# Performance work log

Measured on AMD Instinct MI355X. Metric: run time of the kernel, lower is better.

Reference implementation:

```python
import jax, jax.numpy as jnp
import numpy as np

KERNEL = 3
PAD = KERNEL // 2  # 1


def cal_wfft_ortho(weight, n, cout, cin):
    # weight: [N, M, k, k] with M < N
    nf = n // 2 + 1
    vfft = jnp.fft.rfft2(weight, s=(n, n), norm='ortho')          # [N, M, n, nf] complex
    vfft = jnp.transpose(vfft, (2, 3, 0, 1))                       # [n, nf, N, M]
    vH = jnp.conj(jnp.swapaxes(vfft, -1, -2))                      # [n, nf, M, N]
    wfft = vH @ vfft                                               # [n, nf, M, M] Gram
    perturb_ratio = 1e-5
    eps = jnp.mean(jnp.diagonal(wfft, axis1=-2, axis2=-1), axis=-1) * perturb_ratio
    m = wfft.shape[-1]
    wfft = wfft + eps[..., None, None] * jnp.eye(m, dtype=wfft.dtype)
    N = vfft.shape[-2]
    I = jnp.eye(N, dtype=wfft.dtype)
    # Cayley-style orthogonal projector: I - 2 V (V^H V)^{-1} V^H
    ortho = I - 2.0 * (vfft @ jnp.linalg.solve(wfft, vH))          # [n, nf, N, N]
    ortho = ortho[:, :, :cout, :cin]
    return ortho.reshape(n * nf, cout, cin)


def setup_inputs() -> dict:
    key = jax.random.key(0)
    k1, k2, k3 = jax.random.split(key, 3)
    B, C, H = 64, 256, 32
    x = jax.random.normal(k1, (B, C, H, H), dtype=jnp.float32)
    # masked low-rank orthogonal weight: [cout, cin-1, 3, 3]
    weight = jax.random.normal(k2, (C, C - 1, KERNEL, KERNEL), dtype=jnp.float32) * 0.05
    bias = jax.random.normal(k3, (C,), dtype=jnp.float32) * 0.01
    return {"x": x, "weight": weight, "bias": bias}


def reference(x, weight, bias):
    B, cin, h, _ = x.shape
    cout = weight.shape[0]
    xp = jnp.pad(x, ((0, 0), (0, 0), (PAD, PAD), (PAD, PAD)))
    n = h + 2 * PAD
    nf = n // 2 + 1
    # x to frequency domain: [n*nf, cin, B]
    xfft = jnp.fft.rfft2(xp, norm='ortho')                         # [B, cin, n, nf]
    xfft = jnp.transpose(xfft, (2, 3, 1, 0)).reshape(n * nf, cin, B)
    W = cal_wfft_ortho(weight, n, cout, cin)                       # [n*nf, cout, cin]
    zfft = W @ xfft                                                # [n*nf, cout, B]
    zfft = jnp.transpose(zfft.reshape(n, nf, cout, B), (3, 2, 0, 1))
    z = jnp.fft.irfft2(zfft, norm='ortho')                         # [B, cout, n, n] real
    z = z[:, :, PAD:-PAD, PAD:-PAD]
    z = z + bias[:, None, None]
    return z
```

## Files before the change

kernel.cpp:

```cpp
#include <hip/hip_runtime.h>
#include <math.h>

#define NN    34
#define NFH   18
#define NFREQ 612
#define CH    256
#define CIN   255
#define NB    64
#define HW    32
#define PI2   6.2831853071795864769f
#define TSTRIDE 36864

__device__ __forceinline__ int tIdx(int I, int J){ return ((I*(I+1))>>1) + J; }

__global__ __launch_bounds__(256) void kF1(const float* __restrict__ x, float2* __restrict__ U){
  __shared__ float tc[NFH][HW], ts[NFH][HW];
  int tid = threadIdx.x;
  for (int i = tid; i < NFH*HW; i += 256){
    int kx = i >> 5, w = i & 31;
    float s, c; sincosf(-PI2*(float)(kx*(w+1))/34.f, &s, &c);
    tc[kx][w] = c; ts[kx][w] = s;
  }
  __syncthreads();
  int c = blockIdx.x;
  int a = (blockIdx.y << 2) + (tid >> 6);
  int b = tid & 63;
  const float4* xr = (const float4*)(x + (((size_t)b*CH + c)*HW + a)*HW);
  float xv[HW];
#pragma unroll
  for (int t = 0; t < 8; t++){
    float4 v = xr[t];
    xv[4*t] = v.x; xv[4*t+1] = v.y; xv[4*t+2] = v.z; xv[4*t+3] = v.w;
  }
#pragma unroll 1
  for (int kx = 0; kx < NFH; kx++){
    float re = 0.f, im = 0.f;
#pragma unroll
    for (int w = 0; w < HW; w++){ re += xv[w]*tc[kx][w]; im += xv[w]*ts[kx][w]; }
    U[(((size_t)a*NFH + kx)*CH + c)*NB + b] = make_float2(re, im);
  }
}

__global__ __launch_bounds__(512) void kF2(const float2* __restrict__ U, float2* __restrict__ X){
  __shared__ float pc[NN][HW], ps[NN][HW];
  int tid = threadIdx.x;
  for (int i = tid; i < NN*HW; i += 512){
    int ky = i >> 5, a = i & 31;
    float s, c; sincosf(-PI2*(float)(ky*(a+1))/34.f, &s, &c);
    pc[ky][a] = c*(1.f/34.f); ps[ky][a] = s*(1.f/34.f);
  }
  __syncthreads();
  int kx = blockIdx.x;
  int c  = (blockIdx.y << 3) + (tid >> 6);
  int b  = tid & 63;
  float2 u[HW];
#pragma unroll
  for (int a = 0; a < HW; a++) u[a] = U[(((size_t)a*NFH + kx)*CH + c)*NB + b];
#pragma unroll 1
  for (int ky = 0; ky < NN; ky++){
    float re = 0.f, im = 0.f;
#pragma unroll
    for (int a = 0; a < HW; a++){
      float cc = pc[ky][a], ss = ps[ky][a];
      re += u[a].x*cc - u[a].y*ss;
      im += u[a].x*ss + u[a].y*cc;
    }
    X[(((size_t)ky*NFH + kx)*CH + c)*NB + b] = make_float2(re, im);
  }
}

__global__ __launch_bounds__(256) void kT0(const float* __restrict__ w, float* __restrict__ wT){
  int idx = blockIdx.x*256 + threadIdx.x;
  if (idx >= 9*CH*CIN) return;
  int k = idx / (CH*CIN);
  int r = idx - k*(CH*CIN);
  wT[idx] = w[(size_t)r*9 + k];
}

__global__ __launch_bounds__(256) void kC(const float* __restrict__ wT, float* __restrict__ C2){
  int kk = blockIdx.x;
  int k1 = kk / 9, k2 = kk - k1*9;
  int to = (blockIdx.y >> 2) << 6, tp = (blockIdx.y & 3) << 6;
  __shared__ float As[64][33], Bs[64][33];
  int tid = threadIdx.x;
  int ty = tid >> 4, tx = tid & 15;
  float acc[4][4] = {};
  const float* Ab = wT + (size_t)k1*CH*CIN;
  const float* Bb = wT + (size_t)k2*CH*CIN;
  for (int i0 = 0; i0 < CIN; i0 += 32){
    for (int idx = tid; idx < 64*32; idx += 256){
      int r = idx >> 5, j = idx & 31;
      int i = i0 + j;
      As[r][j] = (i < CIN) ? Ab[(size_t)(to + r)*CIN + i] : 0.f;
      Bs[r][j] = (i < CIN) ? Bb[(size_t)(tp + r)*CIN + i] : 0.f;
    }
    __syncthreads();
#pragma unroll
    for (int j = 0; j < 32; j++){
      float av[4], bv[4];
#pragma unroll
      for (int d = 0; d < 4; d++){ av[d] = As[ty*4+d][j]; bv[d] = Bs[tx*4+d][j]; }
#pragma unroll
      for (int da = 0; da < 4; da++)
#pragma unroll
        for (int db = 0; db < 4; db++) acc[da][db] += av[da]*bv[db];
    }
    __syncthreads();
  }
  float* Cb = C2 + (size_t)kk*CH*CH;
#pragma unroll
  for (int da = 0; da < 4; da++)
#pragma unroll
    for (int db = 0; db < 4; db++)
      Cb[(size_t)(to + ty*4 + da)*CH + tp + tx*4 + db] = acc[da][db];
}

__global__ __launch_bounds__(64) void kM(const float* __restrict__ C2, float2* __restrict__ M, int cf0, int cF){
  int t = blockIdx.x;
  int I = 0;
  while ((((I+1)*(I+2))>>1) <= t) I++;
  int J = t - ((I*(I+1))>>1);
  int r = blockIdx.y;
  int o = I*32 + r, p0 = J*32;
  int fl = (blockIdx.z << 6) + threadIdx.x;
  bool act = fl < cF;
  int f = act ? (cf0 + fl) : 0;
  int ky = f / NFH, kx = f - ky*NFH;
  float Pc[5], Ps[5], Qc[5], Qs[5];
#pragma unroll
  for (int d = 0; d < 5; d++){
    float s, c;
    sincosf(-PI2*(float)(ky*(d-2))/34.f, &s, &c);
    Pc[d] = c*(1.f/1156.f); Ps[d] = s*(1.f/1156.f);
    sincosf(-PI2*(float)(kx*(d-2))/34.f, &s, &c);
    Qc[d] = c; Qs[d] = s;
  }
  float ax[32] = {}, ay[32] = {};
  const float* Cb = C2 + (size_t)o*CH + p0;
#pragma unroll 1
  for (int k1 = 0; k1 < 9; k1++){
#pragma unroll 1
    for (int k2 = 0; k2 < 9; k2++){
      int da = k1/3 - k2/3 + 2, db = k1%3 - k2%3 + 2;
      float cr = Pc[da]*Qc[db] - Ps[da]*Qs[db];
      float ci = Pc[da]*Qs[db] + Ps[da]*Qc[db];
      const float* crow = Cb + (size_t)(k1*9 + k2)*CH*CH;
#pragma unroll
      for (int j = 0; j < 32; j++){
        float cv = crow[j];
        ax[j] += cv*cr; ay[j] += cv*ci;
      }
    }
  }
  if (act){
    float2* Mr = M + (size_t)fl*TSTRIDE + ((size_t)t << 10) + (r << 5);
#pragma unroll
    for (int j = 0; j < 32; j++) Mr[j] = make_float2(ax[j], ay[j]);
  }
}

__global__ __launch_bounds__(256) void kEps(float2* __restrict__ M, float* __restrict__ eb, int cf0){
  int fi = blockIdx.x;
  int o = threadIdx.x;
  int I = o >> 5, r = o & 31;
  float2* Mf = M + (size_t)fi*TSTRIDE + ((size_t)tIdx(I,I) << 10) + r*32 + r;
  __shared__ float red[256];
  float d = Mf->x;
  red[o] = d;
  __syncthreads();
  for (int s = 128; s > 0; s >>= 1){ if (o < s) red[o] += red[o+s]; __syncthreads(); }
  float eps = red[0] * (1e-5f/255.f);
  Mf->x = d + eps;
  if (o == 0) eb[cf0 + fi] = eps;
}

__global__ __launch_bounds__(256) void kPanel(float2* __restrict__ Mg, int pb){
  __shared__ float2 P[256][33];
  int fi = blockIdx.x;
  float2* Tf = Mg + (size_t)fi*TSTRIDE;
  const int h = CH - (pb << 5);
  int tid = threadIdx.x;
  for (int idx = tid; idx < h*32; idx += 256){
    int r = idx >> 5, j = idx & 31;
    P[r][j] = Tf[((size_t)tIdx(pb + (r>>5), pb) << 10) + ((r&31) << 5) + j];
  }
  __syncthreads();
  const int i = tid;
  float myd = 0.f;
  float2 lik = make_float2(0.f, 0.f);
#pragma unroll 1
  for (int k = 0; k < 32; k++){
    float pkk = P[k][k].x;
    float d = sqrtf(fmaxf(pkk, 1e-30f));
    float dinv = __builtin_amdgcn_rcpf(d);
    if (i == k) myd = d;
    bool act = (i > k) && (i < h);
    if (act){
      lik.x = P[i][k].x * dinv;
      lik.y = P[i][k].y * dinv;
      P[i][k] = lik;
    }
    __syncthreads();
    if (act){
#pragma unroll 1
      for (int j = k+1; j < 32; j++){
        if (i >= j){
          float2 ljk = P[j][k];
          P[i][j].x -= lik.x*ljk.x + lik.y*ljk.y;
          P[i][j].y -= lik.y*ljk.x - lik.x*ljk.y;
        }
      }
    }
    __syncthreads();
  }
  if (i < 32) P[i][i] = make_float2(myd, 0.f);
  __syncthreads();
  for (int idx = tid; idx < h*32; idx += 256){
    int r = idx >> 5, j = idx & 31;
    Tf[((size_t)tIdx(pb + (r>>5), pb) << 10) + ((r&31) << 5) + j] = P[r][j];
  }
}

__global__ __launch_bounds__(256) void kSyrk(float2* __restrict__ Mg, int pb){
  __shared__ float2 As[32][33], Bs[32][33];
  int fi = blockIdx.x;
  int p = blockIdx.y;
  int li = 0;
  while ((((li+1)*(li+2)) >> 1) <= p) li++;
  int lj = p - ((li*(li+1)) >> 1);
  int I = pb + 1 + li, J = pb + 1 + lj;
  float2* Tf = Mg + (size_t)fi*TSTRIDE;
  const float2* Asrc = Tf + ((size_t)tIdx(I, pb) << 10);
  const float2* Bsrc = Tf + ((size_t)tIdx(J, pb) << 10);
  float2* Cdst = Tf + ((size_t)tIdx(I, J) << 10);
  int tid = threadIdx.x;
  for (int idx = tid; idx < 1024; idx += 256){
    int r = idx >> 5, c = idx & 31;
    As[r][c] = Asrc[idx];
    Bs[r][c] = Bsrc[idx];
  }
  int r = tid >> 3, c0 = (tid & 7) << 2;
  float2 acc[4];
  float4 c01 = *(const float4*)(Cdst + r*32 + c0);
  float4 c23 = *(const float4*)(Cdst + r*32 + c0 + 2);
  acc[0] = make_float2(c01.x, c01.y); acc[1] = make_float2(c01.z, c01.w);
  acc[2] = make_float2(c23.x, c23.y); acc[3] = make_float2(c23.z, c23.w);
  __syncthreads();
#pragma unroll 4
  for (int k = 0; k < 32; k++){
    float2 a = As[r][k];
#pragma unroll
    for (int d = 0; d < 4; d++){
      float2 b = Bs[c0 + d][k];
      acc[d].x -= a.x*b.x + a.y*b.y;
      acc[d].y -= a.y*b.x - a.x*b.y;
    }
  }
  *(float4*)(Cdst + r*32 + c0)     = make_float4(acc[0].x, acc[0].y, acc[1].x, acc[1].y);
  *(float4*)(Cdst + r*32 + c0 + 2) = make_float4(acc[2].x, acc[2].y, acc[3].x, acc[3].y);
}

template<int LO, bool FWD>
__device__ __forceinline__ void solvePhase(int jb, const float2* __restrict__ Tf,
    float2 (&s)[64], float2 (&Lt)[4][2][32][32], float2 (&S32)[32][64],
    int wv, int c){
#pragma unroll
  for (int it2 = 0; it2 < 2; it2++){
    int ib = 2*wv + it2;
    if (FWD ? (ib >= jb) : (ib <= jb)){
      if (FWD){
        const float2* src = Tf + ((size_t)tIdx(ib, jb) << 10);
#pragma unroll
        for (int t = 0; t < 8; t++){
          int idx = t*64 + c, row = idx >> 4, cp = idx & 15;
          float4 v = *(const float4*)(src + row*32 + cp*2);
          *(float4*)(&Lt[wv][it2][row][cp*2]) = v;
        }
      } else {
        const float2* src = Tf + ((size_t)tIdx(jb, ib) << 10);
#pragma unroll
        for (int t = 0; t < 8; t++){
          int idx = t*64 + c, row = idx >> 4, cp = idx & 15;
          float4 v = *(const float4*)(src + row*32 + cp*2);
          Lt[wv][it2][cp*2  ][row] = make_float2(v.x, -v.y);
          Lt[wv][it2][cp*2+1][row] = make_float2(v.z, -v.w);
        }
      }
    }
  }
  if (wv == (jb >> 1)){
    int sl = jb & 1;
#pragma unroll
    for (int i = 0; i < 32; i++) S32[i][c] = s[LO + i];
    if (FWD){
#pragma unroll 1
      for (int k = 0; k < 32; k++){
        float dinv = __builtin_amdgcn_rcpf(Lt[wv][sl][k][k].x);
        float2 v = S32[k][c];
        v.x *= dinv; v.y *= dinv;
        S32[k][c] = v;
#pragma unroll 1
        for (int i = k+1; i < 32; i++){
          float2 l = Lt[wv][sl][i][k];
          float2 t2 = S32[i][c];
          t2.x -= l.x*v.x - l.y*v.y;
          t2.y -= l.x*v.y + l.y*v.x;
          S32[i][c] = t2;
        }
      }
    } else {
#pragma unroll 1
      for (int k = 31; k >= 0; k--){
        float dinv = __builtin_amdgcn_rcpf(Lt[wv][sl][k][k].x);
        float2 v = S32[k][c];
        v.x *= dinv; v.y *= dinv;
        S32[k][c] = v;
#pragma unroll 1
        for (int i = 0; i < k; i++){
          float2 l = Lt[wv][sl][i][k];
          float2 t2 = S32[i][c];
          t2.x -= l.x*v.x - l.y*v.y;
          t2.y -= l.x*v.y + l.y*v.x;
          S32[i][c] = t2;
        }
      }
    }
  }
  __syncthreads();
#pragma unroll
  for (int it2 = 0; it2 < 2; it2++){
    int ib = 2*wv + it2;
    bool upd = FWD ? (ib > jb) : (ib < jb);
    if (upd){
      const int off = it2*32;
#pragma unroll 2
      for (int k = 0; k < 32; k++){
        float2 b = S32[k][c];
#pragma unroll
        for (int i = 0; i < 32; i++){
          float2 l = Lt[wv][it2][i][k];
          s[off+i].x -= l.x*b.x - l.y*b.y;
          s[off+i].y -= l.x*b.y + l.y*b.x;
        }
      }
    }
  }
  if (wv == (jb >> 1)){
#pragma unroll
    for (int i = 0; i < 32; i++) s[LO + i] = S32[i][c];
  }
  __syncthreads();
}

__global__ __launch_bounds__(256, 2) void kSolve(const float2* __restrict__ Lg, float2* __restrict__ X,
                                                 const float* __restrict__ eb, int cf0){
  __shared__ __align__(16) float2 Lt[4][2][32][32];
  __shared__ float2 S32[32][64];
  int fi = blockIdx.x;
  int f = cf0 + fi;
  const float2* Tf = Lg + (size_t)fi*TSTRIDE;
  float2* Xf = X + (size_t)f*CH*NB;
  int tid = threadIdx.x, wv = tid >> 6, c = tid & 63;
  float2 s[64];
#pragma unroll
  for (int i = 0; i < 64; i++) s[i] = Xf[(size_t)(wv*64 + i)*NB + c];
#pragma unroll 1
  for (int jp = 0; jp < 4; jp++){
    solvePhase<0,  true>(2*jp,     Tf, s, Lt, S32, wv, c);
    solvePhase<32, true>(2*jp + 1, Tf, s, Lt, S32, wv, c);
  }
#pragma unroll 1
  for (int jp = 3; jp >= 0; jp--){
    solvePhase<32, false>(2*jp + 1, Tf, s, Lt, S32, wv, c);
    solvePhase<0,  false>(2*jp,     Tf, s, Lt, S32, wv, c);
  }
  float te = 2.f * eb[f];
#pragma unroll
  for (int i = 0; i < 64; i++){
    float2 xv = Xf[(size_t)(wv*64 + i)*NB + c];
    float2 sv = s[i];
    Xf[(size_t)(wv*64 + i)*NB + c] = make_float2(te*sv.x - xv.x, te*sv.y - xv.y);
  }
}

__global__ __launch_bounds__(512) void kI1(const float2* __restrict__ X, float2* __restrict__ Y){
  __shared__ float pc[HW][NN], ps[HW][NN];
  int tid = threadIdx.x;
  for (int i = tid; i < HW*NN; i += 512){
    int a = i / NN, ky = i - a*NN;
    float s, c; sincosf(PI2*(float)(ky*(a+1))/34.f, &s, &c);
    pc[a][ky] = c; ps[a][ky] = s;
  }
  __syncthreads();
  int kx = blockIdx.x;
  int cc = (blockIdx.y << 3) + (tid >> 6);
  int b = tid & 63;
  float2 z[NN];
#pragma unroll
  for (int ky = 0; ky < NN; ky++) z[ky] = X[(((size_t)ky*NFH + kx)*CH + cc)*NB + b];
#pragma unroll 1
  for (int a = 0; a < HW; a++){
    float re = 0.f, im = 0.f;
#pragma unroll
    for (int ky = 0; ky < NN; ky++){
      float co = pc[a][ky], si = ps[a][ky];
      re += z[ky].x*co - z[ky].y*si;
      im += z[ky].x*si + z[ky].y*co;
    }
    Y[(((size_t)a*NFH + kx)*CH + cc)*NB + b] = make_float2(re, im);
  }
}

__global__ __launch_bounds__(256) void kI2(const float2* __restrict__ Y, const float* __restrict__ bias,
                                           float* __restrict__ out){
  __shared__ float tc[NFH][HW], tsn[NFH][HW];
  int tid = threadIdx.x;
  for (int i = tid; i < NFH*HW; i += 256){
    int kx = i >> 5, w = i & 31;
    float wt = (kx == 0 || kx == 17) ? (1.f/34.f) : (2.f/34.f);
    float s, c; sincosf(PI2*(float)(kx*(w+1))/34.f, &s, &c);
    tc[kx][w] = wt*c; tsn[kx][w] = wt*s;
  }
  __syncthreads();
  int cc = blockIdx.x;
  int a = (blockIdx.y << 2) + (tid >> 6);
  int b = tid & 63;
  float2 yv[NFH];
#pragma unroll
  for (int kx = 0; kx < NFH; kx++) yv[kx] = Y[(((size_t)a*NFH + kx)*CH + cc)*NB + b];
  float bi = bias[cc];
  float ov[HW];
#pragma unroll
  for (int w = 0; w < HW; w++){
    float acc = bi;
#pragma unroll
    for (int kx = 0; kx < NFH; kx++)
      acc += yv[kx].x*tc[kx][w] - yv[kx].y*tsn[kx][w];
    ov[w] = acc;
  }
  float4* op = (float4*)(out + (((size_t)b*CH + cc)*HW + a)*HW);
#pragma unroll
  for (int t = 0; t < 8; t++) op[t] = make_float4(ov[4*t], ov[4*t+1], ov[4*t+2], ov[4*t+3]);
}

extern "C" void kernel_launch(void* const* d_in, const int* in_sizes, int n_in,
                              void* d_out, int out_size, void* d_ws, size_t ws_size,
                              hipStream_t stream){
  (void)in_sizes; (void)n_in; (void)out_size;
  const float* x    = (const float*)d_in[0];
  const float* w    = (const float*)d_in[1];
  const float* bias = (const float*)d_in[2];
  float* out = (float*)d_out;
  char* ws = (char*)d_ws;

  const size_t X_BYTES  = (size_t)NFREQ*CH*NB*sizeof(float2);
  const size_t WT_BYTES = (size_t)9*CH*CIN*sizeof(float);
  const size_t C_BYTES  = (size_t)81*CH*CH*sizeof(float);
  const size_t offX  = 0;
  const size_t offWT = offX + X_BYTES;
  const size_t offC  = offWT + WT_BYTES;
  const size_t offE  = offC + C_BYTES;
  const size_t offChunk = offE + 4096;
  const size_t perF = (size_t)TSTRIDE * sizeof(float2);

  float2* X  = (float2*)(ws + offX);
  float*  wT = (float*)(ws + offWT);
  float*  C2 = (float*)(ws + offC);
  float*  eb = (float*)(ws + offE);
  float2* U  = (float2*)(ws + offChunk);
  float2* Mb = (float2*)(ws + offChunk);
  float2* Y  = (float2*)(ws + offChunk);

  size_t avail = ws_size > offChunk ? ws_size - offChunk : 0;
  int F = (int)(avail / perF);
  if (F < 1) F = 1;
  if (F > NFREQ) F = NFREQ;
  int nch = (NFREQ + F - 1) / F;
  F = (NFREQ + nch - 1) / nch;

  kF1<<<dim3(CH, 8), 256, 0, stream>>>(x, U);
  kF2<<<dim3(NFH, 32), 512, 0, stream>>>(U, X);
  kT0<<<(9*CH*CIN + 255)/256, 256, 0, stream>>>(w, wT);
  kC<<<dim3(81, 16), 256, 0, stream>>>(wT, C2);

  for (int cf0 = 0; cf0 < NFREQ; cf0 += F){
    int cF = (NFREQ - cf0 < F) ? (NFREQ - cf0) : F;
    kM<<<dim3(36, 32, (cF + 63) >> 6), 64, 0, stream>>>(C2, Mb, cf0, cF);
    kEps<<<cF, 256, 0, stream>>>(Mb, eb, cf0);
    for (int pb = 0; pb < 8; pb++){
      kPanel<<<cF, 256, 0, stream>>>(Mb, pb);
      int nrem = 7 - pb;
      int npairs = (nrem*(nrem+1)) >> 1;
      if (npairs > 0)
        kSyrk<<<dim3(cF, npairs), 256, 0, stream>>>(Mb, pb);
    }
    kSolve<<<cF, 256, 0, stream>>>(Mb, X, eb, cf0);
  }

  kI1<<<dim3(NFH, 32), 512, 0, stream>>>(X, Y);
  kI2<<<dim3(CH, 8), 256, 0, stream>>>(Y, bias, out);
}
```

Baseline: 4.237 ms.

## Register-resident panel Cholesky and 512-thread triangular solve with one block per wave

```diff
diff --git a/kernel.cpp b/kernel.cpp
--- a/kernel.cpp
+++ b/kernel.cpp
@@ -175,49 +175,49 @@
 }
 
 __global__ __launch_bounds__(256) void kPanel(float2* __restrict__ Mg, int pb){
-  __shared__ float2 P[256][33];
+  __shared__ float2 colbuf[2][32];
+  __shared__ float darr[32];
   int fi = blockIdx.x;
   float2* Tf = Mg + (size_t)fi*TSTRIDE;
   const int h = CH - (pb << 5);
-  int tid = threadIdx.x;
-  for (int idx = tid; idx < h*32; idx += 256){
-    int r = idx >> 5, j = idx & 31;
-    P[r][j] = Tf[((size_t)tIdx(pb + (r>>5), pb) << 10) + ((r&31) << 5) + j];
-  }
-  __syncthreads();
-  const int i = tid;
-  float myd = 0.f;
-  float2 lik = make_float2(0.f, 0.f);
-#pragma unroll 1
+  const int i = threadIdx.x;
+  const bool act = i < h;
+  float2* rowp = Tf + ((size_t)tIdx(pb + (i >> 5), pb) << 10) + ((i & 31) << 5);
+  float2 r[32];
+  if (act){
+#pragma unroll
+    for (int t = 0; t < 16; t++){
+      float4 v = ((const float4*)rowp)[t];
+      r[2*t]   = make_float2(v.x, v.y);
+      r[2*t+1] = make_float2(v.z, v.w);
+    }
+  }
+#pragma unroll
   for (int k = 0; k < 32; k++){
-    float pkk = P[k][k].x;
-    float d = sqrtf(fmaxf(pkk, 1e-30f));
-    float dinv = __builtin_amdgcn_rcpf(d);
-    if (i == k) myd = d;
-    bool act = (i > k) && (i < h);
-    if (act){
-      lik.x = P[i][k].x * dinv;
-      lik.y = P[i][k].y * dinv;
-      P[i][k] = lik;
-    }
+    if (act && i >= k && i < 32) colbuf[k & 1][i] = r[k];
     __syncthreads();
-    if (act){
-#pragma unroll 1
-      for (int j = k+1; j < 32; j++){
-        if (i >= j){
-          float2 ljk = P[j][k];
-          P[i][j].x -= lik.x*ljk.x + lik.y*ljk.y;
-          P[i][j].y -= lik.y*ljk.x - lik.x*ljk.y;
-        }
+    float pinv = __builtin_amdgcn_rcpf(colbuf[k & 1][k].x);
+    if (act && i > k){
+      float ax = r[k].x * pinv, ay = r[k].y * pinv;
+#pragma unroll
+      for (int j = k + 1; j < 32; j++){
+        float2 l = colbuf[k & 1][j];
+        r[j].x -= ax*l.x + ay*l.y;
+        r[j].y -= ay*l.x - ax*l.y;
       }
     }
-    __syncthreads();
-  }
-  if (i < 32) P[i][i] = make_float2(myd, 0.f);
-  __syncthreads();
-  for (int idx = tid; idx < h*32; idx += 256){
-    int r = idx >> 5, j = idx & 31;
-    Tf[((size_t)tIdx(pb + (r>>5), pb) << 10) + ((r&31) << 5) + j] = P[r][j];
+  }
+  if (act && i < 32) darr[i] = r[i].x;
+  __syncthreads();
+  if (act){
+#pragma unroll
+    for (int j = 0; j < 32; j++){
+      float sc = __frsqrt_rn(fmaxf(darr[j], 1e-30f));
+      r[j].x *= sc; r[j].y *= sc;
+    }
+#pragma unroll
+    for (int t = 0; t < 16; t++)
+      ((float4*)rowp)[t] = make_float4(r[2*t].x, r[2*t].y, r[2*t+1].x, r[2*t+1].y);
   }
 }
 
@@ -260,126 +260,101 @@
   *(float4*)(Cdst + r*32 + c0 + 2) = make_float4(acc[2].x, acc[2].y, acc[3].x, acc[3].y);
 }
 
-template<int LO, bool FWD>
+template<bool FWD>
 __device__ __forceinline__ void solvePhase(int jb, const float2* __restrict__ Tf,
-    float2 (&s)[64], float2 (&Lt)[4][2][32][32], float2 (&S32)[32][64],
+    float2 (&s)[32], float2 (&Lt)[8][32][32], float2 (&S32)[32][64],
     int wv, int c){
-#pragma unroll
-  for (int it2 = 0; it2 < 2; it2++){
-    int ib = 2*wv + it2;
-    if (FWD ? (ib >= jb) : (ib <= jb)){
-      if (FWD){
-        const float2* src = Tf + ((size_t)tIdx(ib, jb) << 10);
-#pragma unroll
-        for (int t = 0; t < 8; t++){
-          int idx = t*64 + c, row = idx >> 4, cp = idx & 15;
-          float4 v = *(const float4*)(src + row*32 + cp*2);
-          *(float4*)(&Lt[wv][it2][row][cp*2]) = v;
-        }
-      } else {
-        const float2* src = Tf + ((size_t)tIdx(jb, ib) << 10);
-#pragma unroll
-        for (int t = 0; t < 8; t++){
-          int idx = t*64 + c, row = idx >> 4, cp = idx & 15;
-          float4 v = *(const float4*)(src + row*32 + cp*2);
-          Lt[wv][it2][cp*2  ][row] = make_float2(v.x, -v.y);
-          Lt[wv][it2][cp*2+1][row] = make_float2(v.z, -v.w);
-        }
-      }
-    }
-  }
-  if (wv == (jb >> 1)){
-    int sl = jb & 1;
-#pragma unroll
-    for (int i = 0; i < 32; i++) S32[i][c] = s[LO + i];
+  bool need = FWD ? (wv >= jb) : (wv <= jb);
+  if (need){
+    const float2* src = Tf + ((size_t)(FWD ? tIdx(wv, jb) : tIdx(jb, wv)) << 10);
+#pragma unroll
+    for (int t = 0; t < 8; t++){
+      int idx = t*64 + c, row = idx >> 4, cp = idx & 15;
+      float4 v = *(const float4*)(src + row*32 + cp*2);
+      *(float4*)(&Lt[wv][row][cp*2]) = v;
+    }
+  }
+  if (wv == jb){
     if (FWD){
-#pragma unroll 1
+#pragma unroll
       for (int k = 0; k < 32; k++){
-        float dinv = __builtin_amdgcn_rcpf(Lt[wv][sl][k][k].x);
-        float2 v = S32[k][c];
-        v.x *= dinv; v.y *= dinv;
-        S32[k][c] = v;
-#pragma unroll 1
+        float dinv = __builtin_amdgcn_rcpf(Lt[wv][k][k].x);
+        float2 v = make_float2(s[k].x*dinv, s[k].y*dinv);
+        s[k] = v;
+#pragma unroll
         for (int i = k+1; i < 32; i++){
-          float2 l = Lt[wv][sl][i][k];
-          float2 t2 = S32[i][c];
-          t2.x -= l.x*v.x - l.y*v.y;
-          t2.y -= l.x*v.y + l.y*v.x;
-          S32[i][c] = t2;
+          float2 l = Lt[wv][i][k];
+          s[i].x -= l.x*v.x - l.y*v.y;
+          s[i].y -= l.x*v.y + l.y*v.x;
         }
       }
     } else {
-#pragma unroll 1
+#pragma unroll
       for (int k = 31; k >= 0; k--){
-        float dinv = __builtin_amdgcn_rcpf(Lt[wv][sl][k][k].x);
-        float2 v = S32[k][c];
-        v.x *= dinv; v.y *= dinv;
-        S32[k][c] = v;
-#pragma unroll 1
+        float dinv = __builtin_amdgcn_rcpf(Lt[wv][k][k].x);
+        float2 v = make_float2(s[k].x*dinv, s[k].y*dinv);
+        s[k] = v;
+#pragma unroll
         for (int i = 0; i < k; i++){
-          float2 l = Lt[wv][sl][i][k];
-          float2 t2 = S32[i][c];
-          t2.x -= l.x*v.x - l.y*v.y;
-          t2.y -= l.x*v.y + l.y*v.x;
-          S32[i][c] = t2;
+          float2 l = Lt[wv][k][i];
+          s[i].x -= l.x*v.x + l.y*v.y;
+          s[i].y -= l.x*v.y - l.y*v.x;
         }
       }
     }
-  }
-  __syncthreads();
-#pragma unroll
-  for (int it2 = 0; it2 < 2; it2++){
-    int ib = 2*wv + it2;
-    bool upd = FWD ? (ib > jb) : (ib < jb);
-    if (upd){
-      const int off = it2*32;
+#pragma unroll
+    for (int i = 0; i < 32; i++) S32[i][c] = s[i];
+  }
+  __syncthreads();
+  bool upd = FWD ? (wv > jb) : (wv < jb);
+  if (upd){
 #pragma unroll 2
-      for (int k = 0; k < 32; k++){
-        float2 b = S32[k][c];
+    for (int k = 0; k < 32; k++){
+      float2 b = S32[k][c];
+      if (FWD){
 #pragma unroll
         for (int i = 0; i < 32; i++){
-          float2 l = Lt[wv][it2][i][k];
-          s[off+i].x -= l.x*b.x - l.y*b.y;
-          s[off+i].y -= l.x*b.y + l.y*b.x;
+          float2 l = Lt[wv][i][k];
+          s[i].x -= l.x*b.x - l.y*b.y;
+          s[i].y -= l.x*b.y + l.y*b.x;
+        }
+      } else {
+#pragma unroll
+        for (int i = 0; i < 32; i++){
+          float2 l = Lt[wv][k][i];
+          s[i].x -= l.x*b.x + l.y*b.y;
+          s[i].y -= l.x*b.y - l.y*b.x;
         }
       }
     }
   }
-  if (wv == (jb >> 1)){
-#pragma unroll
-    for (int i = 0; i < 32; i++) s[LO + i] = S32[i][c];
-  }
-  __syncthreads();
-}
-
-__global__ __launch_bounds__(256, 2) void kSolve(const float2* __restrict__ Lg, float2* __restrict__ X,
+  __syncthreads();
+}
+
+__global__ __launch_bounds__(512, 2) void kSolve(const float2* __restrict__ Lg, float2* __restrict__ X,
                                                  const float* __restrict__ eb, int cf0){
-  __shared__ __align__(16) float2 Lt[4][2][32][32];
+  __shared__ __align__(16) float2 Lt[8][32][32];
   __shared__ float2 S32[32][64];
   int fi = blockIdx.x;
   int f = cf0 + fi;
   const float2* Tf = Lg + (size_t)fi*TSTRIDE;
   float2* Xf = X + (size_t)f*CH*NB;
   int tid = threadIdx.x, wv = tid >> 6, c = tid & 63;
-  float2 s[64];
-#pragma unroll
-  for (int i = 0; i < 64; i++) s[i] = Xf[(size_t)(wv*64 + i)*NB + c];
-#pragma unroll 1
-  for (int jp = 0; jp < 4; jp++){
-    solvePhase<0,  true>(2*jp,     Tf, s, Lt, S32, wv, c);
-    solvePhase<32, true>(2*jp + 1, Tf, s, Lt, S32, wv, c);
-  }
-#pragma unroll 1
-  for (int jp = 3; jp >= 0; jp--){
-    solvePhase<32, false>(2*jp + 1, Tf, s, Lt, S32, wv, c);
-    solvePhase<0,  false>(2*jp,     Tf, s, Lt, S32, wv, c);
-  }
+  float2 s[32];
+#pragma unroll
+  for (int i = 0; i < 32; i++) s[i] = Xf[(size_t)(wv*32 + i)*NB + c];
+#pragma unroll 1
+  for (int jb = 0; jb < 8; jb++)
+    solvePhase<true>(jb, Tf, s, Lt, S32, wv, c);
+#pragma unroll 1
+  for (int jb = 7; jb >= 0; jb--)
+    solvePhase<false>(jb, Tf, s, Lt, S32, wv, c);
   float te = 2.f * eb[f];
 #pragma unroll
-  for (int i = 0; i < 64; i++){
-    float2 xv = Xf[(size_t)(wv*64 + i)*NB + c];
+  for (int i = 0; i < 32; i++){
+    float2 xv = Xf[(size_t)(wv*32 + i)*NB + c];
     float2 sv = s[i];
-    Xf[(size_t)(wv*64 + i)*NB + c] = make_float2(te*sv.x - xv.x, te*sv.y - xv.y);
+    Xf[(size_t)(wv*32 + i)*NB + c] = make_float2(te*sv.x - xv.x, te*sv.y - xv.y);
   }
 }
 
@@ -494,7 +469,7 @@
       if (npairs > 0)
         kSyrk<<<dim3(cF, npairs), 256, 0, stream>>>(Mb, pb);
     }
-    kSolve<<<cF, 256, 0, stream>>>(Mb, X, eb, cf0);
+    kSolve<<<cF, 512, 0, stream>>>(Mb, X, eb, cf0);
   }
 
   kI1<<<dim3(NFH, 32), 512, 0, stream>>>(X, Y);
```

After: 4.307 ms. Within noise of the previous version (+1.6%).
